# Performance work log

Hardware: AMD Instinct MI355X
Metric: run time of the kernel (lower is better)

Reference implementation:

```python
import jax, jax.numpy as jnp
import numpy as np

EPS = 1e-5  # BatchNorm3d default eps


def setup_inputs() -> dict:
    key = jax.random.key(0)
    ks = jax.random.split(key, 8)
    B, C, T, H, W = 2, 256, 8, 28, 28
    P, NS = 128, 5
    sc = 0.02  # keep activations stable through 5 residual stages
    return {
        "x": jax.random.normal(ks[0], (B, C, T, H, W), jnp.float32),
        "Wt": jax.random.normal(ks[1], (P, C), jnp.float32) * sc,
        "Wp": jax.random.normal(ks[2], (P, C), jnp.float32) * sc,
        "Wg": jax.random.normal(ks[3], (NS, P, C), jnp.float32) * sc,
        "W1": jax.random.normal(ks[4], (NS, C, P), jnp.float32) * sc,
        "W2": jax.random.normal(ks[5], (NS, C, P), jnp.float32) * sc,
        "gamma": jnp.ones((NS, C), jnp.float32),
        "beta": jnp.zeros((NS, C), jnp.float32),
    }


def _batchnorm(x, g, b):
    # x: [B, C, S]; training-mode BN over (batch, spatial) per channel
    mu = jnp.mean(x, axis=(0, 2), keepdims=True)
    var = jnp.var(x, axis=(0, 2), keepdims=True)
    xn = (x - mu) * jax.lax.rsqrt(var + EPS)
    return xn * g[None, :, None] + b[None, :, None]


def reference(x, Wt, Wp, Wg, W1, W2, gamma, beta):
    B, C, T, H, W = x.shape
    S = T * H * W
    xf = x.reshape(B, C, S)                      # [B,C,S]
    # DotKernel: att[b,i,j] = softmax_j( t[b,i,:] . p[b,:,j] )
    t = jnp.einsum("bcs,pc->bsp", xf, Wt)        # [B,S,P]
    p = jnp.einsum("bcs,pc->bps", xf, Wp)        # [B,P,S]
    att = jax.nn.softmax(jnp.einsum("bsp,bpq->bsq", t, p), axis=-1)  # [B,S,S]

    out = xf
    n_stages = Wg.shape[0]
    for i in range(n_stages):  # small fixed stage count
        g = jnp.einsum("bcs,pc->bsp", out, Wg[i])          # [B,S,P]
        x1 = jnp.einsum("bsp,cp->bcs", g, W1[i])           # w_1(g)
        x2 = jnp.einsum("bsq,bqp->bsp", att, g)            # att @ g
        x2 = jnp.einsum("bsp,cp->bcs", x2, W2[i])          # w_2(...)
        out = _batchnorm(x1 + x2, gamma[i], beta[i]) + out  # BN + residual
    return out.reshape(B, C, T, H, W)
```

## Files before the change

### kernel.cpp

```cpp
#include <hip/hip_runtime.h>

#define B_  2
#define C_  256
#define S_  6272
#define P_  128
#define NS_ 5
#define KS_ 4
#define KCH_ 1568
#define KY_ 640
#define EPS_ 1e-5f

typedef __attribute__((ext_vector_type(8))) short short8;
typedef __attribute__((ext_vector_type(4))) float f32x4;

__device__ __forceinline__ ushort f2bf(float f) {
    union { float f; unsigned u; } v; v.f = f;
    unsigned r = v.u + 0x7fffu + ((v.u >> 16) & 1u);
    return (ushort)(r >> 16);
}
__device__ __forceinline__ float bf2f(ushort h) {
    union { unsigned u; float f; } v; v.u = ((unsigned)h) << 16;
    return v.f;
}

__device__ __forceinline__ void gload16(const ushort* g, ushort* lds) {
    __builtin_amdgcn_global_load_lds(
        (const __attribute__((address_space(1))) void*)g,
        (__attribute__((address_space(3))) void*)lds, 16, 0, 0);
}

__global__ void k_convert_weights(const float* __restrict__ Wt, const float* __restrict__ Wp,
                                  const float* __restrict__ Wg, const float* __restrict__ W1,
                                  const float* __restrict__ W2,
                                  ushort* __restrict__ Wtpb,
                                  ushort* __restrict__ Wgb, ushort* __restrict__ cat2b,
                                  float* __restrict__ statb) {
    int i = blockIdx.x * 256 + threadIdx.x;
    const int nWtp  = 2 * P_ * C_;
    const int nWg   = NS_ * P_ * C_;
    const int nCat2 = NS_ * C_ * KY_;
    if (i < nWtp) {
        int c = i & (C_ - 1), row = i >> 8;
        float v = (row < P_) ? Wt[row * C_ + c] : Wp[(row - P_) * C_ + c];
        Wtpb[i] = f2bf(v);
    }
    if (i < nWg) { Wgb[i] = f2bf(Wg[i]); }
    if (i < nCat2) {
        int k  = i % KY_;
        int c  = (i / KY_) & (C_ - 1);
        int st = i / (KY_ * C_);
        float v = (k < P_) ? W1[((size_t)st * C_ + c) * P_ + k]
                           : W2[((size_t)st * C_ + c) * P_ + ((k - P_) & (P_ - 1))];
        cat2b[i] = f2bf(v);
    }
    if (i < NS_ * 2 * C_) statb[i] = 0.f;
}

__global__ void k_init_x(const float* __restrict__ x, float* __restrict__ out,
                         ushort* __restrict__ xb_sc) {
    int bc = blockIdx.x;
    int b = bc / C_, c = bc - b * C_;
    const float* xr = x + (long)bc * S_;
    float* orow = out + (long)bc * S_;
    ushort* xs = xb_sc + (long)b * S_ * C_;
    for (int s = threadIdx.x; s < S_; s += 256) {
        float v = xr[s];
        orow[s] = v;
        xs[(long)s * C_ + c] = f2bf(v);
    }
}

template <int MODE>
__global__ __launch_bounds__(256, 2)
void k_gemm(const ushort* __restrict__ A, const ushort* __restrict__ Bm,
            void* __restrict__ Out, ushort* __restrict__ OutT, float* __restrict__ Stat,
            int M, int N, int K, int lda, int ldb, int ldo, int ldot,
            long sA, long sB, long sOb, long sOch, long sOT, int nks, int kch) {
    const int z = blockIdx.z;
    const int b = z / nks, ch = z - b * nks;
    A  += (long)b * sA;
    Bm += (long)b * sB;
    const int k0 = ch * kch, k1 = k0 + kch;

    const int bm = blockIdx.x * 128, bn = blockIdx.y * 128;

    __shared__ ushort Al[128][32];
    __shared__ ushort Bl[128][32];

    const int tid = threadIdx.x, lane = tid & 63, wid = tid >> 6;
    const int wr = (wid >> 1) * 64, wc = (wid & 1) * 64;
    const int r16 = lane & 15, kg = lane >> 4;

    const int st_row = lane >> 2;
    const int st_slot = lane & 3;
    const int st_gk8 = ((st_slot ^ ((st_row >> 1) & 3)) << 3);
    const int sw8 = ((kg ^ ((r16 >> 1) & 3)) << 3);

    const ushort* Arow0 = A + (long)(bm + wid * 32 + st_row) * lda + st_gk8;
    const ushort* Arow1 = A + (long)(bm + wid * 32 + 16 + st_row) * lda + st_gk8;
    const ushort* Brow0 = Bm + (long)(bn + wid * 32 + st_row) * ldb + st_gk8;
    const ushort* Brow1 = Bm + (long)(bn + wid * 32 + 16 + st_row) * ldb + st_gk8;

    f32x4 acc[4][4];
    #pragma unroll
    for (int i = 0; i < 4; ++i)
        #pragma unroll
        for (int j = 0; j < 4; ++j)
            acc[i][j] = (f32x4){0.f, 0.f, 0.f, 0.f};

    for (int kk = k0; kk < k1; kk += 32) {
        gload16(Arow0 + kk, &Al[wid * 32][0]);
        gload16(Arow1 + kk, &Al[wid * 32 + 16][0]);
        gload16(Brow0 + kk, &Bl[wid * 32][0]);
        gload16(Brow1 + kk, &Bl[wid * 32 + 16][0]);
        __syncthreads();

        short8 af[4], bfv[4];
        #pragma unroll
        for (int i = 0; i < 4; ++i)
            af[i] = *(const short8*)&Al[wr + i * 16 + r16][sw8];
        #pragma unroll
        for (int j = 0; j < 4; ++j)
            bfv[j] = *(const short8*)&Bl[wc + j * 16 + r16][sw8];

        #pragma unroll
        for (int i = 0; i < 4; ++i)
            #pragma unroll
            for (int j = 0; j < 4; ++j)
                acc[i][j] = __builtin_amdgcn_mfma_f32_16x16x32_bf16(af[i], bfv[j], acc[i][j], 0, 0, 0);
        __syncthreads();
    }

    const int orow0 = bm + wr + kg * 4;
    const int ocol0 = bn + wc + r16;
    if (MODE == 3) {
        float* O = (float*)Out + (long)b * sOb;
        #pragma unroll
        for (int i = 0; i < 4; ++i)
            #pragma unroll
            for (int j = 0; j < 4; ++j)
                #pragma unroll
                for (int q = 0; q < 4; ++q)
                    O[(long)(orow0 + i * 16 + q) * ldo + (ocol0 + j * 16)] = acc[i][j][q];
        #pragma unroll
        for (int i = 0; i < 4; ++i)
            #pragma unroll
            for (int q = 0; q < 4; ++q) {
                float s1 = acc[i][0][q] + acc[i][1][q] + acc[i][2][q] + acc[i][3][q];
                float s2 = acc[i][0][q] * acc[i][0][q] + acc[i][1][q] * acc[i][1][q]
                         + acc[i][2][q] * acc[i][2][q] + acc[i][3][q] * acc[i][3][q];
                #pragma unroll
                for (int off = 1; off < 16; off <<= 1) {
                    s1 += __shfl_xor(s1, off);
                    s2 += __shfl_xor(s2, off);
                }
                if (r16 == 0) {
                    atomicAdd(&Stat[orow0 + i * 16 + q], s1);
                    atomicAdd(&Stat[M + orow0 + i * 16 + q], s2);
                }
            }
    } else {
        ushort* O = (ushort*)Out + (long)b * sOb + (long)ch * sOch;
        ushort* OT = (MODE == 1) ? (OutT + (long)b * sOT) : nullptr;
        #pragma unroll
        for (int i = 0; i < 4; ++i)
            #pragma unroll
            for (int j = 0; j < 4; ++j)
                #pragma unroll
                for (int q = 0; q < 4; ++q) {
                    ushort h = f2bf(acc[i][j][q]);
                    O[(long)(orow0 + i * 16 + q) * ldo + (ocol0 + j * 16)] = h;
                    if (MODE == 1)
                        OT[(long)(ocol0 + j * 16) * ldot + (orow0 + i * 16 + q)] = h;
                }
    }
}

__global__ __launch_bounds__(256)
void k_softmax(ushort* __restrict__ att) {
    long row = blockIdx.x;
    ushort* r = att + row * (long)S_;
    const int tid = threadIdx.x;
    __shared__ float red1[4];
    __shared__ float red2[4];
    const bool tail = tid < 16;

    short8 u0 = *(const short8*)&r[(0 * 256 + tid) * 8];
    short8 u1 = *(const short8*)&r[(1 * 256 + tid) * 8];
    short8 u2 = *(const short8*)&r[(2 * 256 + tid) * 8];
    short8 u3 = tail ? *(const short8*)&r[(768 + tid) * 8] : short8{0,0,0,0,0,0,0,0};

    float v[32];
    #pragma unroll
    for (int j = 0; j < 8; ++j) {
        v[j]      = bf2f((ushort)u0[j]);
        v[8 + j]  = bf2f((ushort)u1[j]);
        v[16 + j] = bf2f((ushort)u2[j]);
        v[24 + j] = tail ? bf2f((ushort)u3[j]) : -1e30f;
    }
    float mx = -1e30f;
    #pragma unroll
    for (int j = 0; j < 32; ++j) mx = fmaxf(mx, v[j]);
    #pragma unroll
    for (int off = 32; off; off >>= 1) mx = fmaxf(mx, __shfl_xor(mx, off));
    if ((tid & 63) == 0) red1[tid >> 6] = mx;
    __syncthreads();
    mx = fmaxf(fmaxf(red1[0], red1[1]), fmaxf(red1[2], red1[3]));

    float sum = 0.f;
    #pragma unroll
    for (int j = 0; j < 32; ++j) {
        float e = __expf(v[j] - mx);
        v[j] = e;
        sum += e;
    }
    #pragma unroll
    for (int off = 32; off; off >>= 1) sum += __shfl_xor(sum, off);
    if ((tid & 63) == 0) red2[tid >> 6] = sum;
    __syncthreads();
    sum = red2[0] + red2[1] + red2[2] + red2[3];
    float inv = 1.f / sum;

    short8 w0, w1, w2, w3;
    #pragma unroll
    for (int j = 0; j < 8; ++j) {
        w0[j] = (short)f2bf(v[j] * inv);
        w1[j] = (short)f2bf(v[8 + j] * inv);
        w2[j] = (short)f2bf(v[16 + j] * inv);
        w3[j] = (short)f2bf(v[24 + j] * inv);
    }
    *(short8*)&r[(0 * 256 + tid) * 8] = w0;
    *(short8*)&r[(1 * 256 + tid) * 8] = w1;
    *(short8*)&r[(2 * 256 + tid) * 8] = w2;
    if (tail) *(short8*)&r[(768 + tid) * 8] = w3;
}

__global__ __launch_bounds__(256)
void k_bn_apply(const float* __restrict__ y, const float* __restrict__ Stat,
                const float* __restrict__ gamma,
                const float* __restrict__ beta, float* __restrict__ out,
                ushort* __restrict__ xb_sc) {
    int bc = blockIdx.x;
    int b = bc / C_, c = bc - b * C_;
    const float invn = 1.f / (float)(B_ * S_);
    float m = Stat[c] * invn;
    float var = Stat[C_ + c] * invn - m * m;
    float r = rsqrtf(var + EPS_);
    float g = gamma[c], be = beta[c];
    const float* yr = y + (long)bc * S_;
    float* orow = out + (long)bc * S_;
    ushort* xs = xb_sc + (long)b * S_ * C_;
    for (int s = threadIdx.x; s < S_; s += 256) {
        float v = orow[s] + (yr[s] - m) * r * g + be;
        orow[s] = v;
        xs[(long)s * C_ + c] = f2bf(v);
    }
}

extern "C" void kernel_launch(void* const* d_in, const int* in_sizes, int n_in,
                              void* d_out, int out_size, void* d_ws, size_t ws_size,
                              hipStream_t stream) {
    const float* x     = (const float*)d_in[0];
    const float* Wt    = (const float*)d_in[1];
    const float* Wp    = (const float*)d_in[2];
    const float* Wg    = (const float*)d_in[3];
    const float* W1    = (const float*)d_in[4];
    const float* W2    = (const float*)d_in[5];
    const float* gamma = (const float*)d_in[6];
    const float* beta  = (const float*)d_in[7];
    float* out = (float*)d_out;

    char* ws = (char*)d_ws;
    size_t off = 0;
    auto alloc = [&](size_t bytes) -> void* {
        void* p = ws + off;
        off = (off + bytes + 255) & ~(size_t)255;
        return p;
    };
    ushort* att   = (ushort*)alloc((size_t)B_ * S_ * S_ * 2);
    ushort* tpb   = (ushort*)alloc((size_t)B_ * S_ * 256 * 2);
    ushort* gTb   = (ushort*)alloc((size_t)B_ * P_ * S_ * 2);
    ushort* Bcat2 = (ushort*)alloc((size_t)B_ * S_ * KY_ * 2);
    ushort* xbsc  = (ushort*)alloc((size_t)B_ * S_ * C_ * 2);
    float*  y     = (float*)alloc((size_t)B_ * C_ * S_ * 4);
    ushort* Wtpb  = (ushort*)alloc((size_t)2 * P_ * C_ * 2);
    ushort* Wgb   = (ushort*)alloc((size_t)NS_ * P_ * C_ * 2);
    ushort* cat2b = (ushort*)alloc((size_t)NS_ * C_ * KY_ * 2);
    float*  statb = (float*)alloc((size_t)NS_ * 2 * C_ * 4);
    if (off > ws_size) return;

    dim3 blk(256);

    k_convert_weights<<<3200, 256, 0, stream>>>(Wt, Wp, Wg, W1, W2, Wtpb, Wgb, cat2b, statb);
    k_init_x<<<B_ * C_, 256, 0, stream>>>(x, out, xbsc);

    k_gemm<0><<<dim3(S_ / 128, 2, B_), blk, 0, stream>>>(
        xbsc, Wtpb, tpb, nullptr, nullptr, S_, 256, C_, C_, C_, 256, 0,
        (long)S_ * C_, 0, (long)S_ * 256, 0, 0, 1, C_);
    k_gemm<0><<<dim3(S_ / 128, S_ / 128, B_), blk, 0, stream>>>(
        tpb, tpb + 128, att, nullptr, nullptr, S_, S_, P_, 256, 256, S_, 0,
        (long)S_ * 256, (long)S_ * 256, (long)S_ * S_, 0, 0, 1, P_);
    k_softmax<<<B_ * S_, 256, 0, stream>>>(att);

    for (int i = 0; i < NS_; ++i) {
        k_gemm<1><<<dim3(S_ / 128, 1, B_), blk, 0, stream>>>(
            xbsc, Wgb + (size_t)i * P_ * C_, Bcat2, gTb, nullptr,
            S_, P_, C_, C_, C_, KY_, S_,
            (long)S_ * C_, 0, (long)S_ * KY_, 0, (long)P_ * S_, 1, C_);
        k_gemm<0><<<dim3(S_ / 128, 1, B_ * KS_), blk, 0, stream>>>(
            att, gTb, Bcat2 + 128, nullptr, nullptr, S_, P_, S_, S_, S_, KY_, 0,
            (long)S_ * S_, (long)P_ * S_, (long)S_ * KY_, 128, 0, KS_, KCH_);
        k_gemm<3><<<dim3(C_ / 128, S_ / 128, B_), blk, 0, stream>>>(
            cat2b + (size_t)i * C_ * KY_, Bcat2, y, nullptr, statb + (size_t)i * 2 * C_,
            C_, S_, KY_, KY_, KY_, S_, 0,
            0, (long)S_ * KY_, (long)C_ * S_, 0, 0, 1, KY_);
        k_bn_apply<<<B_ * C_, 256, 0, stream>>>(y, statb + (size_t)i * 2 * C_,
                                                gamma + i * C_, beta + i * C_, out, xbsc);
    }
}
```

Measured before the change: 779.2 us.

## Double-buffer GEMM LDS, fp32 split-K reduce, shrink concat K, tile transposes

The GEMM main loop now double-buffers LDS so the next K tile's global-to-LDS loads overlap the current MFMA work, with one barrier per iteration. The att@g split-K now uses 7 chunks and writes fp32 partials, which a new reduce kernel sums into a 256-wide concatenated buffer. The old 640-wide concat, which summed four bf16 partials through the K dimension, is replaced, cutting the final W1/W2 GEMM's K from 640 to 256. The init and BN-apply kernels transpose through padded LDS tiles so the bf16 channel-last writes are coalesced 16-byte stores. The cost is an extra fp32 scratch buffer and reduce launch per stage, plus twice the LDS per GEMM block.

```diff
diff --git a/kernel.cpp b/kernel.cpp
--- a/kernel.cpp
+++ b/kernel.cpp
@@ -5,10 +5,10 @@
 #define S_  6272
 #define P_  128
 #define NS_ 5
-#define KS_ 4
-#define KCH_ 1568
-#define KY_ 640
+#define KS_ 7
+#define KCH_ 896
 #define EPS_ 1e-5f
+#define TPAD 264
 
 typedef __attribute__((ext_vector_type(8))) short short8;
 typedef __attribute__((ext_vector_type(4))) float f32x4;
@@ -33,40 +33,52 @@
                                   const float* __restrict__ Wg, const float* __restrict__ W1,
                                   const float* __restrict__ W2,
                                   ushort* __restrict__ Wtpb,
-                                  ushort* __restrict__ Wgb, ushort* __restrict__ cat2b,
+                                  ushort* __restrict__ Wgb, ushort* __restrict__ catb,
                                   float* __restrict__ statb) {
     int i = blockIdx.x * 256 + threadIdx.x;
-    const int nWtp  = 2 * P_ * C_;
-    const int nWg   = NS_ * P_ * C_;
-    const int nCat2 = NS_ * C_ * KY_;
+    const int nWtp = 2 * P_ * C_;
+    const int nWg  = NS_ * P_ * C_;
+    const int nCat = NS_ * C_ * 2 * P_;
     if (i < nWtp) {
         int c = i & (C_ - 1), row = i >> 8;
         float v = (row < P_) ? Wt[row * C_ + c] : Wp[(row - P_) * C_ + c];
         Wtpb[i] = f2bf(v);
     }
     if (i < nWg) { Wgb[i] = f2bf(Wg[i]); }
-    if (i < nCat2) {
-        int k  = i % KY_;
-        int c  = (i / KY_) & (C_ - 1);
-        int st = i / (KY_ * C_);
+    if (i < nCat) {
+        int k  = i & 255;
+        int c  = (i >> 8) & (C_ - 1);
+        int st = i >> 16;
         float v = (k < P_) ? W1[((size_t)st * C_ + c) * P_ + k]
-                           : W2[((size_t)st * C_ + c) * P_ + ((k - P_) & (P_ - 1))];
-        cat2b[i] = f2bf(v);
+                           : W2[((size_t)st * C_ + c) * P_ + (k - P_)];
+        catb[i] = f2bf(v);
     }
     if (i < NS_ * 2 * C_) statb[i] = 0.f;
 }
 
-__global__ void k_init_x(const float* __restrict__ x, float* __restrict__ out,
-                         ushort* __restrict__ xb_sc) {
-    int bc = blockIdx.x;
-    int b = bc / C_, c = bc - b * C_;
-    const float* xr = x + (long)bc * S_;
-    float* orow = out + (long)bc * S_;
-    ushort* xs = xb_sc + (long)b * S_ * C_;
-    for (int s = threadIdx.x; s < S_; s += 256) {
-        float v = xr[s];
-        orow[s] = v;
-        xs[(long)s * C_ + c] = f2bf(v);
+__global__ __launch_bounds__(256)
+void k_init_x(const float* __restrict__ x, float* __restrict__ out,
+              ushort* __restrict__ xb_sc) {
+    __shared__ ushort tl[64][TPAD];
+    const int bs = blockIdx.x;
+    const int b = bs / 98, s0 = (bs - b * 98) * 64;
+    const int tid = threadIdx.x, sl = tid & 63, cg = tid >> 6;
+    #pragma unroll 4
+    for (int it = 0; it < 64; ++it) {
+        int c = it * 4 + cg;
+        long idx = ((long)b * C_ + c) * S_ + s0 + sl;
+        float v = x[idx];
+        out[idx] = v;
+        tl[sl][c] = f2bf(v);
+    }
+    __syncthreads();
+    ushort* xs = xb_sc + ((long)b * S_ + s0) * C_;
+    #pragma unroll
+    for (int u0 = 0; u0 < 2048; u0 += 256) {
+        int u = u0 + tid;
+        int s = u >> 5, c8 = (u & 31) << 3;
+        short8 w = *(const short8*)&tl[s][c8];
+        *(short8*)&xs[(long)s * C_ + c8] = w;
     }
 }
 
@@ -80,12 +92,12 @@
     const int b = z / nks, ch = z - b * nks;
     A  += (long)b * sA;
     Bm += (long)b * sB;
-    const int k0 = ch * kch, k1 = k0 + kch;
+    const int k0 = ch * kch;
 
     const int bm = blockIdx.x * 128, bn = blockIdx.y * 128;
 
-    __shared__ ushort Al[128][32];
-    __shared__ ushort Bl[128][32];
+    __shared__ ushort Al[2][128][32];
+    __shared__ ushort Bl[2][128][32];
 
     const int tid = threadIdx.x, lane = tid & 63, wid = tid >> 6;
     const int wr = (wid >> 1) * 64, wc = (wid & 1) * 64;
@@ -108,33 +120,43 @@
         for (int j = 0; j < 4; ++j)
             acc[i][j] = (f32x4){0.f, 0.f, 0.f, 0.f};
 
-    for (int kk = k0; kk < k1; kk += 32) {
-        gload16(Arow0 + kk, &Al[wid * 32][0]);
-        gload16(Arow1 + kk, &Al[wid * 32 + 16][0]);
-        gload16(Brow0 + kk, &Bl[wid * 32][0]);
-        gload16(Brow1 + kk, &Bl[wid * 32 + 16][0]);
-        __syncthreads();
-
+    auto stage = [&](int kk, int buf) {
+        gload16(Arow0 + kk, &Al[buf][wid * 32][0]);
+        gload16(Arow1 + kk, &Al[buf][wid * 32 + 16][0]);
+        gload16(Brow0 + kk, &Bl[buf][wid * 32][0]);
+        gload16(Brow1 + kk, &Bl[buf][wid * 32 + 16][0]);
+    };
+    auto compute = [&](int buf) {
         short8 af[4], bfv[4];
         #pragma unroll
         for (int i = 0; i < 4; ++i)
-            af[i] = *(const short8*)&Al[wr + i * 16 + r16][sw8];
+            af[i] = *(const short8*)&Al[buf][wr + i * 16 + r16][sw8];
         #pragma unroll
         for (int j = 0; j < 4; ++j)
-            bfv[j] = *(const short8*)&Bl[wc + j * 16 + r16][sw8];
-
+            bfv[j] = *(const short8*)&Bl[buf][wc + j * 16 + r16][sw8];
         #pragma unroll
         for (int i = 0; i < 4; ++i)
             #pragma unroll
             for (int j = 0; j < 4; ++j)
                 acc[i][j] = __builtin_amdgcn_mfma_f32_16x16x32_bf16(af[i], bfv[j], acc[i][j], 0, 0, 0);
+    };
+
+    const int nt = kch >> 5;
+    stage(k0, 0);
+    __syncthreads();
+    int cur = 0;
+    for (int t = 0; t < nt - 1; ++t) {
+        stage(k0 + (t + 1) * 32, cur ^ 1);
+        compute(cur);
         __syncthreads();
-    }
+        cur ^= 1;
+    }
+    compute(cur);
 
     const int orow0 = bm + wr + kg * 4;
     const int ocol0 = bn + wc + r16;
-    if (MODE == 3) {
-        float* O = (float*)Out + (long)b * sOb;
+    if (MODE == 2 || MODE == 3) {
+        float* O = (float*)Out + (long)b * sOb + (long)ch * sOch;
         #pragma unroll
         for (int i = 0; i < 4; ++i)
             #pragma unroll
@@ -142,23 +164,25 @@
                 #pragma unroll
                 for (int q = 0; q < 4; ++q)
                     O[(long)(orow0 + i * 16 + q) * ldo + (ocol0 + j * 16)] = acc[i][j][q];
-        #pragma unroll
-        for (int i = 0; i < 4; ++i)
+        if (MODE == 3) {
             #pragma unroll
-            for (int q = 0; q < 4; ++q) {
-                float s1 = acc[i][0][q] + acc[i][1][q] + acc[i][2][q] + acc[i][3][q];
-                float s2 = acc[i][0][q] * acc[i][0][q] + acc[i][1][q] * acc[i][1][q]
-                         + acc[i][2][q] * acc[i][2][q] + acc[i][3][q] * acc[i][3][q];
+            for (int i = 0; i < 4; ++i)
                 #pragma unroll
-                for (int off = 1; off < 16; off <<= 1) {
-                    s1 += __shfl_xor(s1, off);
-                    s2 += __shfl_xor(s2, off);
+                for (int q = 0; q < 4; ++q) {
+                    float s1 = acc[i][0][q] + acc[i][1][q] + acc[i][2][q] + acc[i][3][q];
+                    float s2 = acc[i][0][q] * acc[i][0][q] + acc[i][1][q] * acc[i][1][q]
+                             + acc[i][2][q] * acc[i][2][q] + acc[i][3][q] * acc[i][3][q];
+                    #pragma unroll
+                    for (int off = 1; off < 16; off <<= 1) {
+                        s1 += __shfl_xor(s1, off);
+                        s2 += __shfl_xor(s2, off);
+                    }
+                    if (r16 == 0) {
+                        atomicAdd(&Stat[orow0 + i * 16 + q], s1);
+                        atomicAdd(&Stat[M + orow0 + i * 16 + q], s2);
+                    }
                 }
-                if (r16 == 0) {
-                    atomicAdd(&Stat[orow0 + i * 16 + q], s1);
-                    atomicAdd(&Stat[M + orow0 + i * 16 + q], s2);
-                }
-            }
+        }
     } else {
         ushort* O = (ushort*)Out + (long)b * sOb + (long)ch * sOch;
         ushort* OT = (MODE == 1) ? (OutT + (long)b * sOT) : nullptr;
@@ -235,25 +259,50 @@
     if (tail) *(short8*)&r[(768 + tid) * 8] = w3;
 }
 
+__global__ void k_reduce_split(const float* __restrict__ split, ushort* __restrict__ BcatT) {
+    long i = (long)blockIdx.x * 256 + threadIdx.x;
+    if (i >= (long)B_ * S_ * P_) return;
+    int p = (int)(i & (P_ - 1));
+    long sp = i >> 7;
+    int b = (int)(sp / S_);
+    long s = sp - (long)b * S_;
+    const float* base = split + (long)b * KS_ * S_ * P_ + s * P_ + p;
+    float acc = 0.f;
+    #pragma unroll
+    for (int ch = 0; ch < KS_; ++ch) acc += base[(long)ch * S_ * P_];
+    BcatT[((long)b * S_ + s) * 256 + 128 + p] = f2bf(acc);
+}
+
 __global__ __launch_bounds__(256)
 void k_bn_apply(const float* __restrict__ y, const float* __restrict__ Stat,
-                const float* __restrict__ gamma,
-                const float* __restrict__ beta, float* __restrict__ out,
-                ushort* __restrict__ xb_sc) {
-    int bc = blockIdx.x;
-    int b = bc / C_, c = bc - b * C_;
+                const float* __restrict__ gamma, const float* __restrict__ beta,
+                float* __restrict__ out, ushort* __restrict__ xb_sc) {
+    __shared__ ushort tl[64][TPAD];
+    const int bs = blockIdx.x;
+    const int b = bs / 98, s0 = (bs - b * 98) * 64;
+    const int tid = threadIdx.x, sl = tid & 63, cg = tid >> 6;
     const float invn = 1.f / (float)(B_ * S_);
-    float m = Stat[c] * invn;
-    float var = Stat[C_ + c] * invn - m * m;
-    float r = rsqrtf(var + EPS_);
-    float g = gamma[c], be = beta[c];
-    const float* yr = y + (long)bc * S_;
-    float* orow = out + (long)bc * S_;
-    ushort* xs = xb_sc + (long)b * S_ * C_;
-    for (int s = threadIdx.x; s < S_; s += 256) {
-        float v = orow[s] + (yr[s] - m) * r * g + be;
-        orow[s] = v;
-        xs[(long)s * C_ + c] = f2bf(v);
+    #pragma unroll 4
+    for (int it = 0; it < 64; ++it) {
+        int c = it * 4 + cg;
+        float m = Stat[c] * invn;
+        float var = Stat[C_ + c] * invn - m * m;
+        float rs = rsqrtf(var + EPS_);
+        float sc = rs * gamma[c];
+        float sh = beta[c] - m * sc;
+        long idx = ((long)b * C_ + c) * S_ + s0 + sl;
+        float v = out[idx] + y[idx] * sc + sh;
+        out[idx] = v;
+        tl[sl][c] = f2bf(v);
+    }
+    __syncthreads();
+    ushort* xs = xb_sc + ((long)b * S_ + s0) * C_;
+    #pragma unroll
+    for (int u0 = 0; u0 < 2048; u0 += 256) {
+        int u = u0 + tid;
+        int s = u >> 5, c8 = (u & 31) << 3;
+        short8 w = *(const short8*)&tl[s][c8];
+        *(short8*)&xs[(long)s * C_ + c8] = w;
     }
 }
 
@@ -280,19 +329,20 @@
     ushort* att   = (ushort*)alloc((size_t)B_ * S_ * S_ * 2);
     ushort* tpb   = (ushort*)alloc((size_t)B_ * S_ * 256 * 2);
     ushort* gTb   = (ushort*)alloc((size_t)B_ * P_ * S_ * 2);
-    ushort* Bcat2 = (ushort*)alloc((size_t)B_ * S_ * KY_ * 2);
+    ushort* BcatT = (ushort*)alloc((size_t)B_ * S_ * 256 * 2);
     ushort* xbsc  = (ushort*)alloc((size_t)B_ * S_ * C_ * 2);
     float*  y     = (float*)alloc((size_t)B_ * C_ * S_ * 4);
+    float*  split = (float*)alloc((size_t)B_ * KS_ * S_ * P_ * 4);
     ushort* Wtpb  = (ushort*)alloc((size_t)2 * P_ * C_ * 2);
     ushort* Wgb   = (ushort*)alloc((size_t)NS_ * P_ * C_ * 2);
-    ushort* cat2b = (ushort*)alloc((size_t)NS_ * C_ * KY_ * 2);
+    ushort* catb  = (ushort*)alloc((size_t)NS_ * C_ * 256 * 2);
     float*  statb = (float*)alloc((size_t)NS_ * 2 * C_ * 4);
     if (off > ws_size) return;
 
     dim3 blk(256);
 
-    k_convert_weights<<<3200, 256, 0, stream>>>(Wt, Wp, Wg, W1, W2, Wtpb, Wgb, cat2b, statb);
-    k_init_x<<<B_ * C_, 256, 0, stream>>>(x, out, xbsc);
+    k_convert_weights<<<1280, 256, 0, stream>>>(Wt, Wp, Wg, W1, W2, Wtpb, Wgb, catb, statb);
+    k_init_x<<<B_ * 98, 256, 0, stream>>>(x, out, xbsc);
 
     k_gemm<0><<<dim3(S_ / 128, 2, B_), blk, 0, stream>>>(
         xbsc, Wtpb, tpb, nullptr, nullptr, S_, 256, C_, C_, C_, 256, 0,
@@ -304,17 +354,18 @@
 
     for (int i = 0; i < NS_; ++i) {
         k_gemm<1><<<dim3(S_ / 128, 1, B_), blk, 0, stream>>>(
-            xbsc, Wgb + (size_t)i * P_ * C_, Bcat2, gTb, nullptr,
-            S_, P_, C_, C_, C_, KY_, S_,
-            (long)S_ * C_, 0, (long)S_ * KY_, 0, (long)P_ * S_, 1, C_);
-        k_gemm<0><<<dim3(S_ / 128, 1, B_ * KS_), blk, 0, stream>>>(
-            att, gTb, Bcat2 + 128, nullptr, nullptr, S_, P_, S_, S_, S_, KY_, 0,
-            (long)S_ * S_, (long)P_ * S_, (long)S_ * KY_, 128, 0, KS_, KCH_);
+            xbsc, Wgb + (size_t)i * P_ * C_, BcatT, gTb, nullptr,
+            S_, P_, C_, C_, C_, 256, S_,
+            (long)S_ * C_, 0, (long)S_ * 256, 0, (long)P_ * S_, 1, C_);
+        k_gemm<2><<<dim3(S_ / 128, 1, B_ * KS_), blk, 0, stream>>>(
+            att, gTb, split, nullptr, nullptr, S_, P_, S_, S_, S_, P_, 0,
+            (long)S_ * S_, (long)P_ * S_, (long)KS_ * S_ * P_, (long)S_ * P_, 0, KS_, KCH_);
+        k_reduce_split<<<(int)(((long)B_ * S_ * P_ + 255) / 256), 256, 0, stream>>>(split, BcatT);
         k_gemm<3><<<dim3(C_ / 128, S_ / 128, B_), blk, 0, stream>>>(
-            cat2b + (size_t)i * C_ * KY_, Bcat2, y, nullptr, statb + (size_t)i * 2 * C_,
-            C_, S_, KY_, KY_, KY_, S_, 0,
-            0, (long)S_ * KY_, (long)C_ * S_, 0, 0, 1, KY_);
-        k_bn_apply<<<B_ * C_, 256, 0, stream>>>(y, statb + (size_t)i * 2 * C_,
+            catb + (size_t)i * C_ * 256, BcatT, y, nullptr, statb + (size_t)i * 2 * C_,
+            C_, S_, 256, 256, 256, S_, 0,
+            0, (long)S_ * 256, (long)C_ * S_, 0, 0, 1, 256);
+        k_bn_apply<<<B_ * 98, 256, 0, stream>>>(y, statb + (size_t)i * 2 * C_,
                                                 gamma + i * C_, beta + i * C_, out, xbsc);
     }
 }
```

After: 722.5 us. 1.08x faster.
